# Optimization experiments

Hardware: AMD Instinct MI355X
Metric: run time of the kernel (lower is better)

## Reference

```python
import jax, jax.numpy as jnp
import numpy as np

B = 2048   # batch of sampled occupation configurations
L = 64     # nphysical (spatial orbitals / MPS sites)
P = 4      # local physical dimension (2 spin orbitals -> 4 occupations)
D = 128    # MPS bond dimension


def setup_inputs() -> dict:
    key = jax.random.key(0)
    k1, k2, k3, k4 = jax.random.split(key, 4)
    onstate = jax.random.randint(k1, (B, L), 0, P)  # occupation per site
    # flat MPS data buffer reshaped to [site, occupation, Dl, Dr];
    # scale by D**-0.5 so the length-L matrix chain stays O(1).
    site_tensors = jax.random.normal(k2, (L, P, D, D), dtype=jnp.float32) * (D ** -0.5)
    left_vec = jax.random.normal(k3, (D,), dtype=jnp.float32)
    right_vec = jax.random.normal(k4, (D,), dtype=jnp.float32)
    return {
        "onstate": onstate,
        "site_tensors": site_tensors,
        "left_vec": left_vec,
        "right_vec": right_vec,
    }


def reference(onstate, site_tensors, right_vec, left_vec=None, **_ignore):
    # keyword-robust shim not needed; real signature below
    raise NotImplementedError


def reference(onstate, site_tensors, left_vec, right_vec):
    """MPS amplitude: amp[b] = l^T (prod_i A[i, s_{b,i}]) r, evaluated as a
    left-to-right chain of gathered batched vector-matrix products."""
    batch = onstate.shape[0]
    s_seq = onstate.T.astype(jnp.int32)                      # [L, B]
    v0 = jnp.broadcast_to(left_vec, (batch, left_vec.shape[0]))  # [B, D]

    def step(v, inp):
        A_i, s_i = inp            # A_i: [P, D, D], s_i: [B]
        M = A_i[s_i]              # data-dependent gather -> [B, D, D]
        v = jnp.einsum('bd,bde->be', v, M)
        return v, None

    vL, _ = jax.lax.scan(step, v0, (site_tensors, s_seq))
    return vL @ right_vec         # [B] amplitudes
```

## Files before the change

kernel.cpp:

```cpp
#include <hip/hip_runtime.h>
#include <hip/hip_fp16.h>

constexpr int L = 64;
constexpr int P = 4;
constexpr int D = 128;
constexpr int B = 2048;
constexpr int EPW = 16;
constexpr int NG = B / EPW;

using v8h = __attribute__((ext_vector_type(8))) _Float16;
using v4h = __attribute__((ext_vector_type(4))) _Float16;
using v4f = __attribute__((ext_vector_type(4))) float;

constexpr size_t UT_OFF  = 0;
constexpr size_t WT_OFF  = 1048576;
constexpr size_t MTF_OFF = 2097152;
constexpr size_t MTB_OFF = 6291456;

constexpr int VLDS0 = 131072;
constexpr int VLDS1 = 131072 + 4096;
constexpr int PLDS  = 131072 + 8192;
constexpr int SMEM_BYTES = PLDS + L * EPW * 4;

#define WAIT_VM8   0xF78
#define WAIT_VM0   0xF70
#define WAIT_LGKM0 0xC07F

__device__ __forceinline__ void gl2lds16(const void* g, void* l) {
  __builtin_amdgcn_global_load_lds(
      (const __attribute__((address_space(1))) void*)g,
      (__attribute__((address_space(3))) void*)l, 16, 0, 0);
}

__global__ void convert_dual(const float* __restrict__ src,
                             _Float16* __restrict__ mtf,
                             _Float16* __restrict__ mtb) {
  const int mat = blockIdx.x;
  const int site = mat >> 2;
  const int t = threadIdx.x;
  if (site >= 32) {
    const float4* sb = (const float4*)(src + (size_t)mat * 16384);
    _Float16* bb = mtb + (size_t)(mat - 128) * 16384;
#pragma unroll
    for (int it = 0; it < 16; ++it) {
      int idx = t + it * 256;
      float4 f = sb[idx];
      v4h h4 = {(_Float16)f.x, (_Float16)f.y, (_Float16)f.z, (_Float16)f.w};
      *(v4h*)(bb + idx * 4) = h4;
    }
    return;
  }
  const float* sb = src + (size_t)mat * 16384;
  _Float16* fb = mtf + (size_t)mat * 16384;
  const int cl = t & 63;
  const int dg = t >> 6;
#pragma unroll
  for (int ch = 0; ch < 2; ++ch) {
    const int c = ch * 64 + cl;
#pragma unroll
    for (int dh = 0; dh < 4; ++dh) {
      const int d8 = dh * 4 + dg;
      v8h v;
#pragma unroll
      for (int j = 0; j < 8; ++j) v[j] = (_Float16)sb[(d8 * 8 + j) * D + c];
      *(v8h*)(fb + c * D + d8 * 8) = v;
    }
  }
}

__global__ __launch_bounds__(512, 1) void mps_half_chain(
    const int* __restrict__ onstate, const _Float16* __restrict__ mtf,
    const _Float16* __restrict__ mtb, const float* __restrict__ left_vec,
    const float* __restrict__ right_vec, float* __restrict__ ut,
    float* __restrict__ wt) {
  extern __shared__ char smem[];
  const int tid = threadIdx.x;
  const int wave = tid >> 6, lane = tid & 63;
  const int me = lane & 15, q4 = lane >> 4;
  const bool fwd = !(blockIdx.x & 1);
  const int b0 = (blockIdx.x >> 1) * EPW;
  const _Float16* mbase = fwd ? mtf : mtb;
  const float* ivec = fwd ? left_vec : right_vec;
  float* ovec = fwd ? ut : wt;

  int* plds = (int*)(smem + PLDS);
#pragma unroll
  for (int j = 0; j < 2; ++j) {
    int idx = tid + j * 512;
    int e = idx >> 6, i = idx & 63;
    plds[i * EPW + e] = onstate[(b0 + e) * L + i];
  }
  if (tid < 256) {
    int e = tid >> 4, seg = tid & 15;
    _Float16* vp = (_Float16*)(smem + VLDS0) + e * 128 + (seg ^ (e & 7)) * 8;
#pragma unroll
    for (int j = 0; j < 8; ++j) vp[j] = (_Float16)ivec[seg * 8 + j];
  }

  char* wbuf = smem + wave * 16384;

  int soff[8];
#pragma unroll
  for (int i = 0; i < 8; ++i) {
    int u = i * 64 + lane;
    int p = u >> 7, r = u & 127, cl = r >> 3, slot = r & 7;
    soff[i] = p * 32768 + (wave * 16 + cl) * 256 + (slot ^ (cl & 7)) * 16;
  }
  auto stage = [&](int ls, int h, int z) {
    const char* gb = (const char*)mbase + (size_t)ls * 131072 + h * 128;
    char* lb = wbuf + z * 8192;
#pragma unroll
    for (int i = 0; i < 8; ++i) gl2lds16(gb + soff[i], lb + i * 1024);
  };
  auto consume = [&](int h, int z, int pm, const char* vb, v4f& acc) {
    const int s0 = h * 8 + q4, s1 = h * 8 + 4 + q4;
    v8h a0 = *(const v8h*)(vb + me * 256 + (s0 ^ (me & 7)) * 16);
    v8h a1 = *(const v8h*)(vb + me * 256 + (s1 ^ (me & 7)) * 16);
    const char* cb = wbuf + z * 8192;
#pragma unroll
    for (int p = 0; p < P; ++p) {
      const bool isp = (pm == p);
      v8h zf = {};
      v8h am0 = isp ? a0 : zf;
      v8h am1 = isp ? a1 : zf;
      const char* pb = cb + p * 2048 + me * 128;
      v8h bf0 = *(const v8h*)(pb + ((q4) ^ (me & 7)) * 16);
      v8h bf1 = *(const v8h*)(pb + ((4 + q4) ^ (me & 7)) * 16);
      acc = __builtin_amdgcn_mfma_f32_16x16x32_f16(am0, bf0, acc, 0, 0, 0);
      acc = __builtin_amdgcn_mfma_f32_16x16x32_f16(am1, bf1, acc, 0, 0, 0);
    }
  };

  stage(fwd ? 0 : 31, 0, 0);
  __syncthreads();

  const int c0 = wave * 16 + me;
  v4f accL = {0.f, 0.f, 0.f, 0.f};
  for (int site = 0; site < 32; ++site) {
    const int site_g = fwd ? site : 63 - site;
    const int ls     = fwd ? site : 31 - site;
    const int pm = plds[site_g * EPW + me];
    const char* vb = smem + ((site & 1) ? VLDS1 : VLDS0);
    v4f acc = {0.f, 0.f, 0.f, 0.f};

    stage(ls, 1, 1);
    consume(0, 0, pm, vb, acc);

    if (site < 31) {
      const int lsn = fwd ? site + 1 : 30 - site;
      __builtin_amdgcn_sched_barrier(0);
      __builtin_amdgcn_s_waitcnt(WAIT_LGKM0);
      __builtin_amdgcn_sched_barrier(0);
      stage(lsn, 0, 0);
      __builtin_amdgcn_s_waitcnt(WAIT_VM8);
      consume(1, 1, pm, vb, acc);
      _Float16* vn = (_Float16*)(smem + ((site & 1) ? VLDS0 : VLDS1));
#pragma unroll
      for (int r = 0; r < 4; ++r) {
        int e = q4 * 4 + r;
        vn[e * 128 + ((c0 >> 3) ^ (e & 7)) * 8 + (c0 & 7)] = (_Float16)acc[r];
      }
      __syncthreads();
    } else {
      __builtin_amdgcn_s_waitcnt(WAIT_VM0);
      consume(1, 1, pm, vb, acc);
      accL = acc;
    }
  }
#pragma unroll
  for (int r = 0; r < 4; ++r) ovec[c0 * B + b0 + q4 * 4 + r] = accL[r];
}

__global__ void combine_uw(const float* __restrict__ ut,
                           const float* __restrict__ wt,
                           float* __restrict__ out) {
  const int b = blockIdx.x * 256 + threadIdx.x;
  float s = 0.f;
#pragma unroll 8
  for (int d = 0; d < D; ++d) s += ut[d * B + b] * wt[d * B + b];
  out[b] = s;
}

extern "C" void kernel_launch(void* const* d_in, const int* in_sizes, int n_in,
                              void* d_out, int out_size, void* d_ws,
                              size_t ws_size, hipStream_t stream) {
  const int*   onstate      = (const int*)d_in[0];
  const float* site_tensors = (const float*)d_in[1];
  const float* left_vec     = (const float*)d_in[2];
  const float* right_vec    = (const float*)d_in[3];
  float*       out          = (float*)d_out;
  char*        ws           = (char*)d_ws;
  float*       ut           = (float*)(ws + UT_OFF);
  float*       wt           = (float*)(ws + WT_OFF);
  _Float16*    mtf          = (_Float16*)(ws + MTF_OFF);
  _Float16*    mtb          = (_Float16*)(ws + MTB_OFF);

  hipFuncSetAttribute((const void*)mps_half_chain,
                      hipFuncAttributeMaxDynamicSharedMemorySize, SMEM_BYTES);

  convert_dual<<<L * P, 256, 0, stream>>>(site_tensors, mtf, mtb);
  mps_half_chain<<<2 * NG, 512, SMEM_BYTES, stream>>>(
      onstate, mtf, mtb, left_vec, right_vec, ut, wt);
  combine_uw<<<B / 256, 256, 0, stream>>>(ut, wt, out);
}
```

Baseline: 133.6 us.

## Split conversion and combine across more blocks, tighten chain-loop waits and barriers

The fp16 conversion kernel now launches two blocks per matrix, each converting half, to double its parallelism. The combine kernel splits the 128-wide dot product across four waves per block and reduces them in shared memory, using 32 blocks instead of 8. In the chain kernel, __syncthreads is replaced by an explicit lgkm wait plus s_barrier, and extra waitcnt/sched_barrier fences are added around the consume steps. The extra VM wait before the first consume in each site could serialize the prefetch of the second half against compute, so the chain may lose some overlap.

```diff
diff --git a/kernel.cpp b/kernel.cpp
--- a/kernel.cpp
+++ b/kernel.cpp
@@ -35,15 +35,16 @@
 __global__ void convert_dual(const float* __restrict__ src,
                              _Float16* __restrict__ mtf,
                              _Float16* __restrict__ mtb) {
-  const int mat = blockIdx.x;
+  const int mat  = blockIdx.x >> 1;
+  const int half = blockIdx.x & 1;
   const int site = mat >> 2;
   const int t = threadIdx.x;
   if (site >= 32) {
     const float4* sb = (const float4*)(src + (size_t)mat * 16384);
     _Float16* bb = mtb + (size_t)(mat - 128) * 16384;
 #pragma unroll
-    for (int it = 0; it < 16; ++it) {
-      int idx = t + it * 256;
+    for (int it = 0; it < 8; ++it) {
+      int idx = t + (half * 8 + it) * 256;
       float4 f = sb[idx];
       v4h h4 = {(_Float16)f.x, (_Float16)f.y, (_Float16)f.z, (_Float16)f.w};
       *(v4h*)(bb + idx * 4) = h4;
@@ -54,17 +55,14 @@
   _Float16* fb = mtf + (size_t)mat * 16384;
   const int cl = t & 63;
   const int dg = t >> 6;
-#pragma unroll
-  for (int ch = 0; ch < 2; ++ch) {
-    const int c = ch * 64 + cl;
-#pragma unroll
-    for (int dh = 0; dh < 4; ++dh) {
-      const int d8 = dh * 4 + dg;
-      v8h v;
-#pragma unroll
-      for (int j = 0; j < 8; ++j) v[j] = (_Float16)sb[(d8 * 8 + j) * D + c];
-      *(v8h*)(fb + c * D + d8 * 8) = v;
-    }
+  const int c = half * 64 + cl;
+#pragma unroll
+  for (int dh = 0; dh < 4; ++dh) {
+    const int d8 = dh * 4 + dg;
+    v8h v;
+#pragma unroll
+    for (int j = 0; j < 8; ++j) v[j] = (_Float16)sb[(d8 * 8 + j) * D + c];
+    *(v8h*)(fb + c * D + d8 * 8) = v;
   }
 }
 
@@ -131,8 +129,8 @@
     }
   };
 
+  __syncthreads();
   stage(fwd ? 0 : 31, 0, 0);
-  __syncthreads();
 
   const int c0 = wave * 16 + me;
   v4f accL = {0.f, 0.f, 0.f, 0.f};
@@ -144,6 +142,8 @@
     v4f acc = {0.f, 0.f, 0.f, 0.f};
 
     stage(ls, 1, 1);
+    __builtin_amdgcn_s_waitcnt(WAIT_VM8);
+    __builtin_amdgcn_sched_barrier(0);
     consume(0, 0, pm, vb, acc);
 
     if (site < 31) {
@@ -153,6 +153,7 @@
       __builtin_amdgcn_sched_barrier(0);
       stage(lsn, 0, 0);
       __builtin_amdgcn_s_waitcnt(WAIT_VM8);
+      __builtin_amdgcn_sched_barrier(0);
       consume(1, 1, pm, vb, acc);
       _Float16* vn = (_Float16*)(smem + ((site & 1) ? VLDS0 : VLDS1));
 #pragma unroll
@@ -160,9 +161,13 @@
         int e = q4 * 4 + r;
         vn[e * 128 + ((c0 >> 3) ^ (e & 7)) * 8 + (c0 & 7)] = (_Float16)acc[r];
       }
-      __syncthreads();
+      __builtin_amdgcn_sched_barrier(0);
+      __builtin_amdgcn_s_waitcnt(WAIT_LGKM0);
+      __builtin_amdgcn_s_barrier();
+      __builtin_amdgcn_sched_barrier(0);
     } else {
       __builtin_amdgcn_s_waitcnt(WAIT_VM0);
+      __builtin_amdgcn_sched_barrier(0);
       consume(1, 1, pm, vb, acc);
       accL = acc;
     }
@@ -174,11 +179,19 @@
 __global__ void combine_uw(const float* __restrict__ ut,
                            const float* __restrict__ wt,
                            float* __restrict__ out) {
-  const int b = blockIdx.x * 256 + threadIdx.x;
+  __shared__ float red[256];
+  const int t = threadIdx.x;
+  const int b = blockIdx.x * 64 + (t & 63);
+  const int w = t >> 6;
   float s = 0.f;
-#pragma unroll 8
-  for (int d = 0; d < D; ++d) s += ut[d * B + b] * wt[d * B + b];
-  out[b] = s;
+#pragma unroll
+  for (int i = 0; i < 32; ++i) {
+    const int d = w * 32 + i;
+    s += ut[d * B + b] * wt[d * B + b];
+  }
+  red[t] = s;
+  __syncthreads();
+  if (t < 64) out[b] = red[t] + red[t + 64] + red[t + 128] + red[t + 192];
 }
 
 extern "C" void kernel_launch(void* const* d_in, const int* in_sizes, int n_in,
@@ -198,8 +211,8 @@
   hipFuncSetAttribute((const void*)mps_half_chain,
                       hipFuncAttributeMaxDynamicSharedMemorySize, SMEM_BYTES);
 
-  convert_dual<<<L * P, 256, 0, stream>>>(site_tensors, mtf, mtb);
+  convert_dual<<<L * P * 2, 256, 0, stream>>>(site_tensors, mtf, mtb);
   mps_half_chain<<<2 * NG, 512, SMEM_BYTES, stream>>>(
       onstate, mtf, mtb, left_vec, right_vec, ut, wt);
-  combine_uw<<<B / 256, 256, 0, stream>>>(ut, wt, out);
-}
+  combine_uw<<<B / 64, 256, 0, stream>>>(ut, wt, out);
+}
```

Result: faster. 127.7 us (-4.5%).
